# Optimization experiments

Hardware: AMD Instinct MI355X
Metric: run time of the kernel (lower is better)

Reference implementation:

```python
import jax, jax.numpy as jnp
import numpy as np

DIM = 768
NUM_HEADS = 8
HEAD_DIM = DIM // NUM_HEADS


def setup_inputs() -> dict:
    key = jax.random.key(0)
    ks = jax.random.split(key, 5)
    B, N, C = 16, 4096, DIM
    x = jax.random.normal(ks[0], (B, N, C), dtype=jnp.float32)
    # nn.Linear(dim, dim*3): weight [3C, C], bias [3C]
    w_qkv = jax.random.normal(ks[1], (3 * C, C), dtype=jnp.float32) * (C ** -0.5)
    b_qkv = jax.random.normal(ks[2], (3 * C,), dtype=jnp.float32) * 0.02
    w_proj = jax.random.normal(ks[3], (C, C), dtype=jnp.float32) * (C ** -0.5)
    b_proj = jax.random.normal(ks[4], (C,), dtype=jnp.float32) * 0.02
    return {"x": x, "w_qkv": w_qkv, "b_qkv": b_qkv, "w_proj": w_proj, "b_proj": b_proj}


def reference(x, w_qkv, b_qkv, w_proj, b_proj):
    B, N, C = x.shape
    H, D = NUM_HEADS, C // NUM_HEADS
    # qkv projection: [B,N,3C] -> [3,B,H,N,D]
    qkv = x @ w_qkv.T + b_qkv
    qkv = qkv.reshape(B, N, 3, H, D).transpose(2, 0, 3, 1, 4)
    q, k, v = qkv[0], qkv[1], qkv[2]
    # dynamic_scale=True: scale by N^-0.5
    q = q * (N ** -0.5)
    # channel attention: contract over tokens N -> [B,H,D,D]
    attn = jnp.einsum("bhnd,bhne->bhde", q, k)
    attn = jax.nn.softmax(attn, axis=-1)
    # (attn @ v^T)^T -> [B,H,N,D]
    out = jnp.einsum("bhde,bhne->bhnd", attn, v)
    out = out.transpose(0, 2, 1, 3).reshape(B, N, C)
    return out @ w_proj.T + b_proj
```

## Files before the change

kernel.cpp:

```cpp
#include <hip/hip_runtime.h>
#include <hip/hip_bf16.h>
#include <stdint.h>

typedef __bf16 bf16;
typedef __bf16 bf16x8 __attribute__((ext_vector_type(8)));
typedef __bf16 bf16x4 __attribute__((ext_vector_type(4)));
typedef float f32x4 __attribute__((ext_vector_type(4)));

__device__ __forceinline__ void gl_lds16(const bf16* g, bf16* l) {
  __builtin_amdgcn_global_load_lds(
      (const __attribute__((address_space(1))) void*)g,
      (__attribute__((address_space(3))) void*)l, 16, 0, 0);
}

__global__ void cvt_f32_bf16(const float* __restrict__ in, bf16* __restrict__ out, int n4) {
  int i = blockIdx.x * blockDim.x + threadIdx.x;
  if (i < n4) {
    float4 v = ((const float4*)in)[i];
    bf16x4 o;
    o[0] = (bf16)v.x; o[1] = (bf16)v.y; o[2] = (bf16)v.z; o[3] = (bf16)v.w;
    ((bf16x4*)out)[i] = o;
  }
}


template<int OP, int HALF>
__device__ __forceinline__ void stage_half(const bf16* __restrict__ G, long r0, int k0,
                                           int K, bf16* ldsOp, int w, int lane) {
#pragma unroll
  for (int j = 0; j < 2; ++j) {
    int rr8 = (w * 2 + j) * 8;
    int rb = (OP == 0) ? ((rr8 & 63) + ((rr8 >> 6) << 7) + HALF * 64)
                       : ((rr8 & 31) + ((rr8 >> 5) << 6) + HALF * 32);
    int row = rb + (lane >> 3);
    int ci = (lane & 7) ^ (row & 7);
    gl_lds16(G + (r0 + row) * (long)K + k0 + ci * 8, ldsOp + rb * 64);
  }
}

#define AF(buf_, mi_, ksel_) (*(const bf16x8*)&lds[buf_][0][aoff0 + (mi_) * 1024 + (ksel_)])
#define BF(buf_, ni_, ksel_) (*(const bf16x8*)&lds[buf_][1][boff0 + (ni_) * 1024 + (ksel_)])
#define MFMA16(a_, b_, c_) c_ = __builtin_amdgcn_mfma_f32_16x16x32_bf16(a_, b_, c_, 0, 0, 0)

#define TILE(t_, buf_) do {                                                         \
    bf16x8 af[4][2], bl[2][2], bh[2][2];                                            \
                                   \
    _Pragma("unroll") for (int mi = 0; mi < 4; mi++) {                              \
      af[mi][0] = AF(buf_, mi, ks0); af[mi][1] = AF(buf_, mi, ks1); }               \
    _Pragma("unroll") for (int ni = 0; ni < 2; ni++) {                              \
      bl[ni][0] = BF(buf_, ni, ks0); bl[ni][1] = BF(buf_, ni, ks1); }               \
    if ((t_) + 1 < T) stage_half<1, 0>(B, n0, ((t_) + 1) * 64, K,                   \
                                       &lds[(buf_) ^ 1][1][0], w, lane);            \
    __builtin_amdgcn_s_barrier();                                                   \
    asm volatile("s_waitcnt lgkmcnt(0)" ::: "memory");                              \
    __builtin_amdgcn_s_setprio(1);                                                  \
    _Pragma("unroll") for (int mi = 0; mi < 4; mi++)                                \
      _Pragma("unroll") for (int ni = 0; ni < 2; ni++) {                            \
        MFMA16(af[mi][0], bl[ni][0], acc[mi][ni]);                                  \
        MFMA16(af[mi][1], bl[ni][1], acc[mi][ni]); }                                \
    __builtin_amdgcn_s_setprio(0);                                                  \
    __builtin_amdgcn_s_barrier();                                                   \
                                          \
    _Pragma("unroll") for (int ni = 0; ni < 2; ni++) {                              \
      bh[ni][0] = BF(buf_, 2 + ni, ks0); bh[ni][1] = BF(buf_, 2 + ni, ks1); }       \
    if ((t_) + 2 < T) stage_half<0, 0>(A, m0, ((t_) + 2) * 64, K,                   \
                                       &lds[buf_][0][0], w, lane);                  \
    __builtin_amdgcn_s_barrier();                                                   \
    asm volatile("s_waitcnt lgkmcnt(0)" ::: "memory");                              \
    __builtin_amdgcn_s_setprio(1);                                                  \
    _Pragma("unroll") for (int mi = 0; mi < 4; mi++)                                \
      _Pragma("unroll") for (int ni = 0; ni < 2; ni++) {                            \
        MFMA16(af[mi][0], bh[ni][0], acc[mi][2 + ni]);                              \
        MFMA16(af[mi][1], bh[ni][1], acc[mi][2 + ni]); }                            \
    __builtin_amdgcn_s_setprio(0);                                                  \
    __builtin_amdgcn_s_barrier();                                                   \
                                          \
    _Pragma("unroll") for (int mi = 0; mi < 4; mi++) {                              \
      af[mi][0] = AF(buf_, 4 + mi, ks0); af[mi][1] = AF(buf_, 4 + mi, ks1); }       \
    if ((t_) + 2 < T) stage_half<1, 1>(B, n0, ((t_) + 2) * 64, K,                   \
                                       &lds[buf_][1][0], w, lane);                  \
    __builtin_amdgcn_s_barrier();                                                   \
    asm volatile("s_waitcnt lgkmcnt(0)" ::: "memory");                              \
    __builtin_amdgcn_s_setprio(1);                                                  \
    _Pragma("unroll") for (int mi = 0; mi < 4; mi++)                                \
      _Pragma("unroll") for (int ni = 0; ni < 2; ni++) {                            \
        MFMA16(af[mi][0], bh[ni][0], acc[4 + mi][2 + ni]);                          \
        MFMA16(af[mi][1], bh[ni][1], acc[4 + mi][2 + ni]); }                        \
    __builtin_amdgcn_s_setprio(0);                                                  \
    __builtin_amdgcn_s_barrier();                                                   \
                             \
    if ((t_) + 2 < T) stage_half<0, 1>(A, m0, ((t_) + 2) * 64, K,                   \
                                       &lds[buf_][0][0], w, lane);                  \
    if ((t_) >= T - 2) { asm volatile("s_waitcnt vmcnt(0)" ::: "memory"); }         \
    else               { asm volatile("s_waitcnt vmcnt(6)" ::: "memory"); }         \
    __builtin_amdgcn_s_barrier();                                                   \
    __builtin_amdgcn_s_setprio(1);                                                  \
    _Pragma("unroll") for (int mi = 0; mi < 4; mi++)                                \
      _Pragma("unroll") for (int ni = 0; ni < 2; ni++) {                            \
        MFMA16(af[mi][0], bl[ni][0], acc[4 + mi][ni]);                              \
        MFMA16(af[mi][1], bl[ni][1], acc[4 + mi][ni]); }                            \
    __builtin_amdgcn_s_setprio(0);                                                  \
    __builtin_amdgcn_s_barrier();                                                   \
  } while (0)

template<int EPI>
__global__ __launch_bounds__(512, 2) void gemm256(
    const bf16* __restrict__ A, const bf16* __restrict__ B,
    const float* __restrict__ bias, void* __restrict__ Cout,
    int N, int K, int nbn, int nwg)
{
  __shared__ __align__(16) bf16 lds[2][2][256 * 64];
  int bid = blockIdx.x;
  int swz = (bid & 7) * (nwg >> 3) + (bid >> 3);
  long m0 = (long)(swz / nbn) * 256;
  int n0i = (swz % nbn) * 256;
  long n0 = n0i;
  int t = threadIdx.x;
  int w = t >> 6, lane = t & 63;
  int wm = w >> 2, wn = w & 3;
  int l16 = lane & 15, quad = lane >> 4;
  int s7 = l16 & 7;
  int aoff0 = (wm * 128 + l16) * 64;
  int boff0 = (wn * 64 + l16) * 64;
  int ks0 = (quad ^ s7) * 8;
  int ks1 = ((4 + quad) ^ s7) * 8;
  const int T = K >> 6;

  f32x4 acc[8][4] = {};

  stage_half<0, 0>(A, m0, 0, K, &lds[0][0][0], w, lane);
  stage_half<1, 1>(B, n0, 0, K, &lds[0][1][0], w, lane);
  stage_half<0, 1>(A, m0, 0, K, &lds[0][0][0], w, lane);
  stage_half<1, 0>(B, n0, 0, K, &lds[0][1][0], w, lane);
  stage_half<0, 0>(A, m0, 64, K, &lds[1][0][0], w, lane);
  stage_half<1, 1>(B, n0, 64, K, &lds[1][1][0], w, lane);
  stage_half<0, 1>(A, m0, 64, K, &lds[1][0][0], w, lane);
  asm volatile("s_waitcnt vmcnt(6)" ::: "memory");
  __builtin_amdgcn_s_barrier();

  for (int tt = 0; tt < T; tt += 2) {
    TILE(tt, 0);
    TILE(tt + 1, 1);
  }

  long crow0 = m0 + wm * 128 + quad * 4;
  int ccol0 = n0i + wn * 64 + l16;
#pragma unroll
  for (int mi = 0; mi < 8; mi++) {
#pragma unroll
    for (int ni = 0; ni < 4; ni++) {
      int col = ccol0 + ni * 16;
      float bv = bias[col];
#pragma unroll
      for (int r = 0; r < 4; r++) {
        float v = acc[mi][ni][r] + bv;
        long row = crow0 + mi * 16 + r;
        if (EPI == 0) {
          if (col < 768) v *= 0.015625f;
          ((bf16*)Cout)[row * (long)N + col] = (bf16)v;
        } else {
          ((float*)Cout)[row * (long)N + col] = v;
        }
      }
    }
  }
}

__global__ __launch_bounds__(256) void attn_qk(const bf16* __restrict__ qkv, float* __restrict__ part)
{
  __shared__ __align__(16) bf16 sQ[96 * 72];
  __shared__ __align__(16) bf16 sK[96 * 72];
  int bh = blockIdx.x >> 1, kb = blockIdx.x & 1;
  int b = bh >> 3, h = bh & 7;
  int t = threadIdx.x;
  int wave = t >> 6, lane = t & 63;
  int wm = wave >> 1, wn = wave & 1;
  int l16 = lane & 15, quad = lane >> 4;
  f32x4 acc[3][3] = {};
  const bf16* Qb = qkv + (long)b * 4096 * 2304 + h * 96;
  const bf16* Kb = Qb + 768;

  for (int it = 0; it < 32; it++) {
    int tok0 = kb * 2048 + it * 64;
    __syncthreads();
#pragma unroll
    for (int i = 0; i < 3; i++) {
      int id = i * 256 + t;
      int tl = id / 12, cc = id % 12;
      uint4 q4 = *(const uint4*)(Qb + (long)(tok0 + tl) * 2304 + cc * 8);
      uint4 k4 = *(const uint4*)(Kb + (long)(tok0 + tl) * 2304 + cc * 8);
      const bf16* qe = (const bf16*)&q4;
      const bf16* ke = (const bf16*)&k4;
#pragma unroll
      for (int j = 0; j < 8; j++) {
        sQ[(cc * 8 + j) * 72 + tl] = qe[j];
        sK[(cc * 8 + j) * 72 + tl] = ke[j];
      }
    }
    __syncthreads();
#pragma unroll
    for (int ks = 0; ks < 2; ks++) {
      bf16x8 af[3], bfr[3];
#pragma unroll
      for (int mi = 0; mi < 3; mi++)
        af[mi] = *(const bf16x8*)&sQ[(wm * 48 + mi * 16 + l16) * 72 + ks * 32 + quad * 8];
#pragma unroll
      for (int ni = 0; ni < 3; ni++)
        bfr[ni] = *(const bf16x8*)&sK[(wn * 48 + ni * 16 + l16) * 72 + ks * 32 + quad * 8];
#pragma unroll
      for (int mi = 0; mi < 3; mi++)
#pragma unroll
        for (int ni = 0; ni < 3; ni++)
          acc[mi][ni] = __builtin_amdgcn_mfma_f32_16x16x32_bf16(af[mi], bfr[ni], acc[mi][ni], 0, 0, 0);
    }
  }
  float* pout = part + (long)(bh * 2 + kb) * 9216;
#pragma unroll
  for (int mi = 0; mi < 3; mi++)
#pragma unroll
    for (int ni = 0; ni < 3; ni++) {
      int row = wm * 48 + mi * 16 + quad * 4;
      int col = wn * 48 + ni * 16 + l16;
#pragma unroll
      for (int r = 0; r < 4; r++)
        pout[(row + r) * 96 + col] = acc[mi][ni][r];
    }
}

__global__ __launch_bounds__(256) void softmax_attn(const float* __restrict__ part, bf16* __restrict__ attn)
{
  __shared__ float s[96 * 97];
  int bh = blockIdx.x;
  int t = threadIdx.x;
  const float* p0 = part + (long)bh * 2 * 9216;
  const float* p1 = p0 + 9216;
  for (int e = t; e < 9216; e += 256) {
    int r = e / 96, c = e % 96;
    s[r * 97 + c] = p0[e] + p1[e];
  }
  __syncthreads();
  if (t < 96) {
    float m = -1e30f;
    for (int i = 0; i < 96; i++) m = fmaxf(m, s[t * 97 + i]);
    float sum = 0.f;
    for (int i = 0; i < 96; i++) {
      float ev = __expf(s[t * 97 + i] - m);
      s[t * 97 + i] = ev;
      sum += ev;
    }
    float inv = 1.f / sum;
    bf16* ao = attn + (long)bh * 9216 + t * 96;
    for (int i = 0; i < 96; i++) ao[i] = (bf16)(s[t * 97 + i] * inv);
  }
}

__global__ __launch_bounds__(256) void attn_v(
    const bf16* __restrict__ qkv, const bf16* __restrict__ attn, bf16* __restrict__ out2)
{
  __shared__ __align__(16) bf16 sV[128 * 96];
  __shared__ __align__(16) bf16 sAt[96 * 96];
  int bh = blockIdx.x >> 5, tb = blockIdx.x & 31;
  int b = bh >> 3, h = bh & 7;
  int tok0 = tb * 128;
  int t = threadIdx.x;
  int wave = t >> 6, lane = t & 63;
  int wm = wave >> 1, wn = wave & 1;
  int l16 = lane & 15, quad = lane >> 4;
  f32x4 acc[4][3] = {};
  const bf16* Vb = qkv + (long)b * 4096 * 2304 + 1536 + h * 96;

#pragma unroll
  for (int j = 0; j < 6; j++) {
    int c = wave * 6 + j;
    int g = c * 64 + lane;
    int tok = g / 12, cc = g % 12;
    gl_lds16(Vb + (long)(tok0 + tok) * 2304 + cc * 8, &sV[c * 512]);
  }
  for (int c = wave; c < 18; c += 4) {
    int g = c * 64 + lane;
    int d = g / 12, cc = g % 12;
    gl_lds16(attn + (long)bh * 9216 + d * 96 + cc * 8, &sAt[c * 512]);
  }
  __syncthreads();
#pragma unroll
  for (int ks = 0; ks < 3; ks++) {
    bf16x8 af[4], bfr[3];
#pragma unroll
    for (int mi = 0; mi < 4; mi++)
      af[mi] = *(const bf16x8*)&sV[(wm * 64 + mi * 16 + l16) * 96 + ks * 32 + quad * 8];
#pragma unroll
    for (int ni = 0; ni < 3; ni++)
      bfr[ni] = *(const bf16x8*)&sAt[(wn * 48 + ni * 16 + l16) * 96 + ks * 32 + quad * 8];
#pragma unroll
    for (int mi = 0; mi < 4; mi++)
#pragma unroll
      for (int ni = 0; ni < 3; ni++)
        acc[mi][ni] = __builtin_amdgcn_mfma_f32_16x16x32_bf16(af[mi], bfr[ni], acc[mi][ni], 0, 0, 0);
  }
  bf16* ob = out2 + (long)(b * 4096 + tok0) * 768 + h * 96;
#pragma unroll
  for (int mi = 0; mi < 4; mi++)
#pragma unroll
    for (int ni = 0; ni < 3; ni++) {
      int row = wm * 64 + mi * 16 + quad * 4;
      int col = wn * 48 + ni * 16 + l16;
#pragma unroll
      for (int r = 0; r < 4; r++)
        ob[(long)(row + r) * 768 + col] = (bf16)acc[mi][ni][r];
    }
}

extern "C" void kernel_launch(void* const* d_in, const int* in_sizes, int n_in,
                              void* d_out, int out_size, void* d_ws, size_t ws_size,
                              hipStream_t stream) {
  const float* x      = (const float*)d_in[0];
  const float* w_qkv  = (const float*)d_in[1];
  const float* b_qkv  = (const float*)d_in[2];
  const float* w_proj = (const float*)d_in[3];
  const float* b_proj = (const float*)d_in[4];

  char* ws = (char*)d_ws;
  bf16*  Xb     = (bf16*)ws;
  bf16*  Wqkvb  = (bf16*)(ws + 100663296);
  bf16*  Wprojb = (bf16*)(ws + 104202240);
  bf16*  qkvb   = (bf16*)(ws + 105381888);
  float* part   = (float*)(ws + 407371776);
  bf16*  attnb  = (bf16*)(ws + 416808960);
  bf16*  out2   = (bf16*)ws;

  cvt_f32_bf16<<<(12582912 + 255) / 256, 256, 0, stream>>>(x, Xb, 12582912);
  cvt_f32_bf16<<<(442368 + 255) / 256, 256, 0, stream>>>(w_qkv, Wqkvb, 442368);
  cvt_f32_bf16<<<(147456 + 255) / 256, 256, 0, stream>>>(w_proj, Wprojb, 147456);

  gemm256<0><<<2304, 512, 0, stream>>>(Xb, Wqkvb, b_qkv, qkvb, 2304, 768, 9, 2304);
  attn_qk<<<256, 256, 0, stream>>>(qkvb, part);
  softmax_attn<<<128, 256, 0, stream>>>(part, attnb);
  attn_v<<<4096, 256, 0, stream>>>(qkvb, attnb, out2);
  gemm256<1><<<768, 512, 0, stream>>>(out2, Wprojb, b_proj, d_out, 768, 768, 3, 768);
}
```

Measured before the change: 819.7 us.

## Write Q/K transposed from QKV GEMM and pipeline attn_qk with async LDS loads

```diff
diff --git a/kernel.cpp b/kernel.cpp
--- a/kernel.cpp
+++ b/kernel.cpp
@@ -106,7 +106,7 @@
 template<int EPI>
 __global__ __launch_bounds__(512, 2) void gemm256(
     const bf16* __restrict__ A, const bf16* __restrict__ B,
-    const float* __restrict__ bias, void* __restrict__ Cout,
+    const float* __restrict__ bias, void* __restrict__ Cout, void* __restrict__ Cout2,
     int N, int K, int nbn, int nwg)
 {
   __shared__ __align__(16) bf16 lds[2][2][256 * 64];
@@ -145,76 +145,116 @@
 
   long crow0 = m0 + wm * 128 + quad * 4;
   int ccol0 = n0i + wn * 64 + l16;
-#pragma unroll
-  for (int mi = 0; mi < 8; mi++) {
-#pragma unroll
-    for (int ni = 0; ni < 4; ni++) {
-      int col = ccol0 + ni * 16;
-      float bv = bias[col];
-#pragma unroll
-      for (int r = 0; r < 4; r++) {
-        float v = acc[mi][ni][r] + bv;
-        long row = crow0 + mi * 16 + r;
-        if (EPI == 0) {
-          if (col < 768) v *= 0.015625f;
-          ((bf16*)Cout)[row * (long)N + col] = (bf16)v;
-        } else {
-          ((float*)Cout)[row * (long)N + col] = v;
+  if (EPI == 0) {
+    if (n0i < 1536) {
+      long bidx = m0 >> 12;
+      long tokb = (m0 & 4095) + wm * 128 + quad * 4;
+      bf16* qkT = (bf16*)Cout;
+#pragma unroll
+      for (int ni = 0; ni < 4; ni++) {
+        int col = ccol0 + ni * 16;
+        float bv = bias[col];
+        float sc = (col < 768) ? 0.015625f : 1.0f;
+#pragma unroll
+        for (int mi = 0; mi < 8; mi++) {
+          bf16x4 pk;
+#pragma unroll
+          for (int r = 0; r < 4; r++) pk[r] = (bf16)((acc[mi][ni][r] + bv) * sc);
+          *(bf16x4*)&qkT[(bidx * 1536 + col) * 4096 + tokb + mi * 16] = pk;
         }
       }
-    }
-  }
-}
-
-__global__ __launch_bounds__(256) void attn_qk(const bf16* __restrict__ qkv, float* __restrict__ part)
+    } else {
+      bf16* Vb = (bf16*)Cout2;
+#pragma unroll
+      for (int mi = 0; mi < 8; mi++) {
+#pragma unroll
+        for (int ni = 0; ni < 4; ni++) {
+          int col = ccol0 + ni * 16;
+          float bv = bias[col];
+          int colv = col - 1536;
+#pragma unroll
+          for (int r = 0; r < 4; r++) {
+            long row = crow0 + mi * 16 + r;
+            Vb[row * 768 + colv] = (bf16)(acc[mi][ni][r] + bv);
+          }
+        }
+      }
+    }
+  } else {
+#pragma unroll
+    for (int mi = 0; mi < 8; mi++) {
+#pragma unroll
+      for (int ni = 0; ni < 4; ni++) {
+        int col = ccol0 + ni * 16;
+        float bv = bias[col];
+#pragma unroll
+        for (int r = 0; r < 4; r++) {
+          long row = crow0 + mi * 16 + r;
+          ((float*)Cout)[row * (long)N + col] = acc[mi][ni][r] + bv;
+        }
+      }
+    }
+  }
+}
+
+__global__ __launch_bounds__(256) void attn_qk(const bf16* __restrict__ qkT, float* __restrict__ part)
 {
-  __shared__ __align__(16) bf16 sQ[96 * 72];
-  __shared__ __align__(16) bf16 sK[96 * 72];
-  int bh = blockIdx.x >> 1, kb = blockIdx.x & 1;
+  __shared__ __align__(16) bf16 sQ[2][96 * 64];
+  __shared__ __align__(16) bf16 sK[2][96 * 64];
+  int s = blockIdx.x & 7, bh = blockIdx.x >> 3;
   int b = bh >> 3, h = bh & 7;
   int t = threadIdx.x;
-  int wave = t >> 6, lane = t & 63;
-  int wm = wave >> 1, wn = wave & 1;
+  int w = t >> 6, lane = t & 63;
+  int wm = w >> 1, wn = w & 1;
   int l16 = lane & 15, quad = lane >> 4;
+  int s7 = l16 & 7;
+  int ks0 = (quad ^ s7) * 8, ks1 = ((4 + quad) ^ s7) * 8;
+  int wb = t & ~63;
   f32x4 acc[3][3] = {};
-  const bf16* Qb = qkv + (long)b * 4096 * 2304 + h * 96;
-  const bf16* Kb = Qb + 768;
-
-  for (int it = 0; it < 32; it++) {
-    int tok0 = kb * 2048 + it * 64;
-    __syncthreads();
-#pragma unroll
-    for (int i = 0; i < 3; i++) {
-      int id = i * 256 + t;
-      int tl = id / 12, cc = id % 12;
-      uint4 q4 = *(const uint4*)(Qb + (long)(tok0 + tl) * 2304 + cc * 8);
-      uint4 k4 = *(const uint4*)(Kb + (long)(tok0 + tl) * 2304 + cc * 8);
-      const bf16* qe = (const bf16*)&q4;
-      const bf16* ke = (const bf16*)&k4;
-#pragma unroll
-      for (int j = 0; j < 8; j++) {
-        sQ[(cc * 8 + j) * 72 + tl] = qe[j];
-        sK[(cc * 8 + j) * 72 + tl] = ke[j];
-      }
-    }
-    __syncthreads();
+  const bf16* Arow = qkT + ((long)b * 1536 + h * 96) * 4096 + s * 512;
+  const bf16* Brow = Arow + (long)768 * 4096;
+
+  auto stage = [&](int buf, int k0) {
+#pragma unroll
+    for (int j = 0; j < 3; j++) {
+      int g = j * 256 + t;
+      int row = g >> 3;
+      int ci = (g & 7) ^ (row & 7);
+      int db = (j * 256 + wb) * 8;
+      gl_lds16(Arow + (long)row * 4096 + k0 + ci * 8, &sQ[buf][db]);
+      gl_lds16(Brow + (long)row * 4096 + k0 + ci * 8, &sK[buf][db]);
+    }
+  };
+
+  stage(0, 0);
+  for (int it = 0; it < 8; it++) {
+    if (it < 7) {
+      stage((it + 1) & 1, (it + 1) * 64);
+      asm volatile("s_waitcnt vmcnt(6)" ::: "memory");
+    } else {
+      asm volatile("s_waitcnt vmcnt(0)" ::: "memory");
+    }
+    __builtin_amdgcn_s_barrier();
+    int buf = it & 1;
 #pragma unroll
     for (int ks = 0; ks < 2; ks++) {
+      int ksel = ks ? ks1 : ks0;
       bf16x8 af[3], bfr[3];
 #pragma unroll
       for (int mi = 0; mi < 3; mi++)
-        af[mi] = *(const bf16x8*)&sQ[(wm * 48 + mi * 16 + l16) * 72 + ks * 32 + quad * 8];
+        af[mi] = *(const bf16x8*)&sQ[buf][(wm * 48 + mi * 16 + l16) * 64 + ksel];
 #pragma unroll
       for (int ni = 0; ni < 3; ni++)
-        bfr[ni] = *(const bf16x8*)&sK[(wn * 48 + ni * 16 + l16) * 72 + ks * 32 + quad * 8];
+        bfr[ni] = *(const bf16x8*)&sK[buf][(wn * 48 + ni * 16 + l16) * 64 + ksel];
 #pragma unroll
       for (int mi = 0; mi < 3; mi++)
 #pragma unroll
         for (int ni = 0; ni < 3; ni++)
           acc[mi][ni] = __builtin_amdgcn_mfma_f32_16x16x32_bf16(af[mi], bfr[ni], acc[mi][ni], 0, 0, 0);
     }
-  }
-  float* pout = part + (long)(bh * 2 + kb) * 9216;
+    __builtin_amdgcn_s_barrier();
+  }
+  float* pout = part + ((long)bh * 8 + s) * 9216;
 #pragma unroll
   for (int mi = 0; mi < 3; mi++)
 #pragma unroll
@@ -232,11 +272,13 @@
   __shared__ float s[96 * 97];
   int bh = blockIdx.x;
   int t = threadIdx.x;
-  const float* p0 = part + (long)bh * 2 * 9216;
-  const float* p1 = p0 + 9216;
+  const float* p0 = part + (long)bh * 8 * 9216;
   for (int e = t; e < 9216; e += 256) {
     int r = e / 96, c = e % 96;
-    s[r * 97 + c] = p0[e] + p1[e];
+    float v = 0.f;
+#pragma unroll
+    for (int s2 = 0; s2 < 8; s2++) v += p0[s2 * 9216 + e];
+    s[r * 97 + c] = v;
   }
   __syncthreads();
   if (t < 96) {
@@ -255,7 +297,7 @@
 }
 
 __global__ __launch_bounds__(256) void attn_v(
-    const bf16* __restrict__ qkv, const bf16* __restrict__ attn, bf16* __restrict__ out2)
+    const bf16* __restrict__ Vb, const bf16* __restrict__ attn, bf16* __restrict__ out2)
 {
   __shared__ __align__(16) bf16 sV[128 * 96];
   __shared__ __align__(16) bf16 sAt[96 * 96];
@@ -267,14 +309,14 @@
   int wm = wave >> 1, wn = wave & 1;
   int l16 = lane & 15, quad = lane >> 4;
   f32x4 acc[4][3] = {};
-  const bf16* Vb = qkv + (long)b * 4096 * 2304 + 1536 + h * 96;
+  const bf16* Vbase = Vb + ((long)b * 4096 + tok0) * 768 + h * 96;
 
 #pragma unroll
   for (int j = 0; j < 6; j++) {
     int c = wave * 6 + j;
     int g = c * 64 + lane;
     int tok = g / 12, cc = g % 12;
-    gl_lds16(Vb + (long)(tok0 + tok) * 2304 + cc * 8, &sV[c * 512]);
+    gl_lds16(Vbase + (long)tok * 768 + cc * 8, &sV[c * 512]);
   }
   for (int c = wave; c < 18; c += 4) {
     int g = c * 64 + lane;
@@ -321,20 +363,21 @@
 
   char* ws = (char*)d_ws;
   bf16*  Xb     = (bf16*)ws;
+  float* part   = (float*)ws;
+  bf16*  out2   = (bf16*)ws;
   bf16*  Wqkvb  = (bf16*)(ws + 100663296);
   bf16*  Wprojb = (bf16*)(ws + 104202240);
-  bf16*  qkvb   = (bf16*)(ws + 105381888);
-  float* part   = (float*)(ws + 407371776);
-  bf16*  attnb  = (bf16*)(ws + 416808960);
-  bf16*  out2   = (bf16*)ws;
+  bf16*  qkT    = (bf16*)(ws + 105381888);
+  bf16*  Vb     = (bf16*)(ws + 306708480);
+  bf16*  attnb  = (bf16*)(ws + 407371776);
 
   cvt_f32_bf16<<<(12582912 + 255) / 256, 256, 0, stream>>>(x, Xb, 12582912);
   cvt_f32_bf16<<<(442368 + 255) / 256, 256, 0, stream>>>(w_qkv, Wqkvb, 442368);
   cvt_f32_bf16<<<(147456 + 255) / 256, 256, 0, stream>>>(w_proj, Wprojb, 147456);
 
-  gemm256<0><<<2304, 512, 0, stream>>>(Xb, Wqkvb, b_qkv, qkvb, 2304, 768, 9, 2304);
-  attn_qk<<<256, 256, 0, stream>>>(qkvb, part);
+  gemm256<0><<<2304, 512, 0, stream>>>(Xb, Wqkvb, b_qkv, qkT, Vb, 2304, 768, 9, 2304);
+  attn_qk<<<1024, 256, 0, stream>>>(qkT, part);
   softmax_attn<<<128, 256, 0, stream>>>(part, attnb);
-  attn_v<<<4096, 256, 0, stream>>>(qkvb, attnb, out2);
-  gemm256<1><<<768, 512, 0, stream>>>(out2, Wprojb, b_proj, d_out, 768, 768, 3, 768);
-}
+  attn_v<<<4096, 256, 0, stream>>>(Vb, attnb, out2);
+  gemm256<1><<<768, 512, 0, stream>>>(out2, Wprojb, b_proj, d_out, nullptr, 768, 768, 3, 768);
+}
```

After: 786.8 us. 1.04x faster.
